# Optimization experiments

Measured on AMD Instinct MI355X. Metric: run time of the kernel, lower is better.

The kernel has to match this reference:

```python
import jax, jax.numpy as jnp
import numpy as np
import math

H = 1024      # hidden_size
NH = 16       # num_attention_heads
HD = H // NH  # head_dim = 64
FF = 4096     # intermediate_size
AD = 256      # adapter_hidden_size
NB = 320      # num_buckets
MAXD = 800    # max_bucket_distance
B = 4
S = 1024
EPS = 1e-5


def _rel_bucket(rel):
    # HF WavLM _relative_positions_bucket
    nb = NB // 2
    buckets = (rel > 0).astype(jnp.int32) * nb
    rel = jnp.abs(rel)
    max_exact = nb // 2
    is_small = rel < max_exact
    large = max_exact + (
        jnp.log(jnp.maximum(rel, 1).astype(jnp.float32) / max_exact)
        / math.log(MAXD / max_exact) * (nb - max_exact)
    ).astype(jnp.int32)
    large = jnp.minimum(large, nb - 1)
    return buckets + jnp.where(is_small, rel, large)


def _ln(x, g, b):
    m = x.mean(-1, keepdims=True)
    v = ((x - m) ** 2).mean(-1, keepdims=True)
    return (x - m) * jax.lax.rsqrt(v + EPS) * g + b


def setup_inputs() -> dict:
    key = jax.random.key(0)
    ks = jax.random.split(key, 12)
    sc = 0.02
    w = lambda k, shape: jax.random.normal(k, shape, jnp.float32) * sc
    return dict(
        x=jax.random.normal(ks[0], (B, S, H), jnp.float32),
        Wq=w(ks[1], (H, H)), bq=jnp.zeros((H,), jnp.float32),
        Wk=w(ks[2], (H, H)), bk=jnp.zeros((H,), jnp.float32),
        Wv=w(ks[3], (H, H)), bv=jnp.zeros((H,), jnp.float32),
        Wo=w(ks[4], (H, H)), bo=jnp.zeros((H,), jnp.float32),
        Wg=w(ks[5], (8, HD)), bg=jnp.zeros((8,), jnp.float32),
        gru_const=jnp.ones((1, NH, 1, 1), jnp.float32),
        rel_embed=w(ks[6], (NB, NH)),
        ln1_g=jnp.ones((H,), jnp.float32), ln1_b=jnp.zeros((H,), jnp.float32),
        W1=w(ks[7], (FF, H)), b1=jnp.zeros((FF,), jnp.float32),
        W2=w(ks[8], (H, FF)), b2=jnp.zeros((H,), jnp.float32),
        ln2_g=jnp.ones((H,), jnp.float32), ln2_b=jnp.zeros((H,), jnp.float32),
        Wad=w(ks[9], (AD, H)), bad=jnp.zeros((AD,), jnp.float32),
        Wau=w(ks[10], (H, AD)), bau=jnp.zeros((H,), jnp.float32),
    )


def reference(x, Wq, bq, Wk, bk, Wv, bv, Wo, bo, Wg, bg, gru_const, rel_embed,
              ln1_g, ln1_b, W1, b1, W2, b2, ln2_g, ln2_b, Wad, bad, Wau, bau):
    b, s, _ = x.shape
    # --- relative position bias (first layer: position_bias=None) ---
    pos = jnp.arange(s)
    rel = pos[None, :] - pos[:, None]                 # memory - context
    pos_bias = rel_embed[_rel_bucket(rel)].transpose(2, 0, 1)  # (nh, s, s)

    # --- GRU-style gating of the bias (per batch, head, query pos) ---
    xh = x.reshape(b, s, NH, HD).transpose(0, 2, 1, 3)         # (b, nh, s, hd)
    gproj = jnp.einsum('bhsd,ed->bhse', xh, Wg) + bg           # (b, nh, s, 8)
    gproj = gproj.reshape(b, NH, s, 2, 4).sum(-1)              # (b, nh, s, 2)
    gate = jax.nn.sigmoid(gproj)
    gate_a, gate_b = gate[..., 0:1], gate[..., 1:2]            # (b, nh, s, 1)
    gate_out = gate_a * (gate_b * gru_const - 1.0) + 2.0       # (b, nh, s, 1)
    gated_bias = gate_out * pos_bias[None]                     # (b, nh, s, s)

    # --- multi-head self-attention with additive gated bias ---
    q = (x @ Wq.T + bq).reshape(b, s, NH, HD)
    k = (x @ Wk.T + bk).reshape(b, s, NH, HD)
    v = (x @ Wv.T + bv).reshape(b, s, NH, HD)
    scores = jnp.einsum('bihd,bjhd->bhij', q, k) * (HD ** -0.5) + gated_bias
    attn = jax.nn.softmax(scores, axis=-1)
    ctx = jnp.einsum('bhij,bjhd->bihd', attn, v).reshape(b, s, H)
    attn_out = ctx @ Wo.T + bo

    # --- residual + LN, FFN + adapter (idx_without_adapter=None path) + LN ---
    h = _ln(x + attn_out, ln1_g, ln1_b)
    ff = jax.nn.gelu(h @ W1.T + b1, approximate=False) @ W2.T + b2
    adapt = jax.nn.elu(h @ Wad.T + bad) @ Wau.T + bau
    h = h + ff + adapt
    return _ln(h, ln2_g, ln2_b)
```

## Files before the change

kernel.cpp:

```cpp
#include <hip/hip_runtime.h>
#include <cmath>

typedef unsigned short u16;
using short8 = __attribute__((ext_vector_type(8))) short;
using f32x4  = __attribute__((ext_vector_type(4))) float;

__device__ __forceinline__ u16 f2bf(float f) {
  union { float f; unsigned u; } c; c.f = f;
  unsigned r = c.u + 0x7fffu + ((c.u >> 16) & 1u);
  return (u16)(r >> 16);
}

__device__ __forceinline__ void gld_lds16(void* lds, const void* g) {
  __builtin_amdgcn_global_load_lds(
      (const __attribute__((address_space(1))) void*)g,
      (__attribute__((address_space(3))) void*)lds, 16, 0, 0);
}

__global__ __launch_bounds__(256) void cvt_bf16(const float* __restrict__ in,
                                                u16* __restrict__ out, int n4) {
  int i = blockIdx.x * 256 + threadIdx.x;
  if (i >= n4) return;
  float4 v = ((const float4*)in)[i];
  ushort4 o;
  o.x = f2bf(v.x); o.y = f2bf(v.y); o.z = f2bf(v.z); o.w = f2bf(v.w);
  ((ushort4*)out)[i] = o;
}

__global__ __launch_bounds__(256) void btab_kernel(const float* __restrict__ rel_embed,
                                                   float* __restrict__ btab) {
  int idx = blockIdx.x * 256 + threadIdx.x;
  if (idx >= 16 * 2048) return;
  int h = idx >> 11;
  int d = idx & 2047;
  if (d >= 2047) return;
  int rel = d - 1023;
  int bucket = (rel > 0) ? 160 : 0;
  int ar = rel < 0 ? -rel : rel;
  if (ar < 80) {
    bucket += ar;
  } else {
    int large = 80 + (int)(logf((float)ar / 80.0f) / 2.3025851f * 80.0f);
    if (large > 159) large = 159;
    bucket += large;
  }
  btab[h * 2048 + d] = rel_embed[bucket * 16 + h];
}

__global__ __launch_bounds__(256) void gate_kernel(const float* __restrict__ x,
                                                   const float* __restrict__ Wg,
                                                   const float* __restrict__ bg,
                                                   const float* __restrict__ gc,
                                                   float* __restrict__ gate_out) {
  int gw = blockIdx.x * 4 + (threadIdx.x >> 6);
  int lane = threadIdx.x & 63;
  int s = gw & 1023, bh = gw >> 10, b = bh >> 4, h = bh & 15;
  float wA = Wg[lane] + Wg[64 + lane] + Wg[128 + lane] + Wg[192 + lane];
  float wB = Wg[256 + lane] + Wg[320 + lane] + Wg[384 + lane] + Wg[448 + lane];
  float xv = x[((size_t)(b * 1024 + s)) * 1024 + h * 64 + lane];
  float pa = xv * wA, pb = xv * wB;
  #pragma unroll
  for (int m = 1; m < 64; m <<= 1) {
    pa += __shfl_xor(pa, m, 64);
    pb += __shfl_xor(pb, m, 64);
  }
  if (lane == 0) {
    float bgA = bg[0] + bg[1] + bg[2] + bg[3];
    float bgB = bg[4] + bg[5] + bg[6] + bg[7];
    float ga = 1.f / (1.f + expf(-(pa + bgA)));
    float gb = 1.f / (1.f + expf(-(pb + bgB)));
    gate_out[(size_t)bh * 1024 + s] = ga * (gb * gc[h] - 1.f) + 2.f;
  }
}

template <int MODE>
__global__ __launch_bounds__(256) void gemm_bt(
    const u16* __restrict__ A, const u16* __restrict__ Bw,
    int M, int N, int K,
    const float* __restrict__ bias0, const float* __restrict__ bias1,
    const float* __restrict__ bias2, const float* __restrict__ resid,
    float* __restrict__ outf,
    u16* __restrict__ ob0, u16* __restrict__ ob1, u16* __restrict__ ob2) {
  __shared__ __align__(16) u16 As[128 * 32];
  __shared__ __align__(16) u16 Bs[128 * 32];
  const int tid = threadIdx.x;
  const int lane = tid & 63, wave = tid >> 6;
  const int quad = lane >> 4, l16 = lane & 15;
  const int bm = blockIdx.y * 128, bn = blockIdx.x * 128;
  const int wm = (wave & 1) * 64, wn = (wave >> 1) * 64;
  const int srow = lane >> 2;
  const int scol = (lane & 3) * 8;

  f32x4 acc[4][4] = {};

  for (int k0 = 0; k0 < K; k0 += 32) {
    #pragma unroll
    for (int it = 0; it < 2; ++it) {
      int rbase = (it * 4 + wave) * 16;
      gld_lds16(&As[rbase * 32], &A[(size_t)(bm + rbase + srow) * K + k0 + scol]);
      gld_lds16(&Bs[rbase * 32], &Bw[(size_t)(bn + rbase + srow) * K + k0 + scol]);
    }
    __syncthreads();
    short8 af[4], bf[4];
    #pragma unroll
    for (int mi = 0; mi < 4; ++mi)
      af[mi] = *(const short8*)&As[(wm + mi * 16 + l16) * 32 + quad * 8];
    #pragma unroll
    for (int ni = 0; ni < 4; ++ni)
      bf[ni] = *(const short8*)&Bs[(wn + ni * 16 + l16) * 32 + quad * 8];
    #pragma unroll
    for (int mi = 0; mi < 4; ++mi)
      #pragma unroll
      for (int ni = 0; ni < 4; ++ni)
        acc[mi][ni] = __builtin_amdgcn_mfma_f32_16x16x32_bf16(af[mi], bf[ni], acc[mi][ni], 0, 0, 0);
    __syncthreads();
  }

  #pragma unroll
  for (int mi = 0; mi < 4; ++mi) {
    #pragma unroll
    for (int ni = 0; ni < 4; ++ni) {
      int col = bn + wn + ni * 16 + l16;
      #pragma unroll
      for (int r = 0; r < 4; ++r) {
        int m = bm + wm + mi * 16 + quad * 4 + r;
        float v = acc[mi][ni][r];
        if constexpr (MODE == 0) {
          int seg = col >> 10;
          int nloc = col & 1023;
          const float* bs = seg == 0 ? bias0 : (seg == 1 ? bias1 : bias2);
          u16* dst = seg == 0 ? ob0 : (seg == 1 ? ob1 : ob2);
          v += bs[nloc];
          if (seg == 0) v *= 0.125f;
          dst[(size_t)m * 1024 + nloc] = f2bf(v);
        } else if constexpr (MODE == 1) {
          v += bias0[col] + resid[(size_t)m * N + col];
          outf[(size_t)m * N + col] = v;
        } else {
          if (col < 4096) {
            float t = v + bias0[col];
            float g = 0.5f * t * (1.f + erff(t * 0.70710678118f));
            ob0[(size_t)m * 4096 + col] = f2bf(g);
          } else {
            int nloc = col - 4096;
            float t = v + bias1[nloc];
            float e = t > 0.f ? t : expm1f(t);
            ob1[(size_t)m * 256 + nloc] = f2bf(e);
          }
        }
      }
    }
  }
}

__global__ __launch_bounds__(256) void attn_kernel(
    const u16* __restrict__ qb, const u16* __restrict__ kb, const u16* __restrict__ vb,
    const float* __restrict__ gate, const float* __restrict__ btab,
    u16* __restrict__ ctxb) {
  __shared__ __align__(16) u16 Qs[64 * 64];
  __shared__ __align__(16) u16 Ks[64 * 64];
  __shared__ __align__(16) u16 Vt[64 * 72];
  __shared__ __align__(16) u16 Ps[4][16 * 72];
  __shared__ float btl[2047];
  __shared__ float gbuf[64];

  const int tid = threadIdx.x;
  const int lane = tid & 63, wave = tid >> 6;
  const int quad = lane >> 4, l16 = lane & 15;
  const int it0 = blockIdx.x * 64;
  const int bh = blockIdx.y, b = bh >> 4, h = bh & 15;

  for (int idx = tid; idx < 2047; idx += 256) btl[idx] = btab[h * 2048 + idx];
  if (tid < 64) gbuf[tid] = gate[(size_t)bh * 1024 + it0 + tid];

  {
    int r = tid >> 3, c = (tid & 7) * 8;
    #pragma unroll
    for (int p = 0; p < 2; ++p) {
      int row = p * 32 + r;
      *(uint4*)&Qs[row * 64 + c] =
          *(const uint4*)&qb[((size_t)(b * 1024 + it0 + row)) * 1024 + h * 64 + c];
    }
  }

  f32x4 oacc[4] = {};
  float mrow[4], lrow[4];
  #pragma unroll
  for (int r = 0; r < 4; ++r) { mrow[r] = -1e30f; lrow[r] = 0.f; }

  __syncthreads();

  for (int jt = 0; jt < 16; ++jt) {
    int j0 = jt * 64;
    {
      int r = tid >> 3, c = (tid & 7) * 8;
      #pragma unroll
      for (int p = 0; p < 2; ++p) {
        int row = p * 32 + r;
        size_t gidx = ((size_t)(b * 1024 + j0 + row)) * 1024 + h * 64 + c;
        *(uint4*)&Ks[row * 64 + c] = *(const uint4*)&kb[gidx];
        uint4 vv = *(const uint4*)&vb[gidx];
        const u16* pv = (const u16*)&vv;
        #pragma unroll
        for (int e = 0; e < 8; ++e) Vt[(c + e) * 72 + row] = pv[e];
      }
    }
    __syncthreads();

    f32x4 sacc[4] = {};
    #pragma unroll
    for (int c = 0; c < 2; ++c) {
      short8 aq = *(const short8*)&Qs[(wave * 16 + l16) * 64 + c * 32 + quad * 8];
      #pragma unroll
      for (int nt = 0; nt < 4; ++nt) {
        short8 bk8 = *(const short8*)&Ks[(nt * 16 + l16) * 64 + c * 32 + quad * 8];
        sacc[nt] = __builtin_amdgcn_mfma_f32_16x16x32_bf16(aq, bk8, sacc[nt], 0, 0, 0);
      }
    }

    float sc[4][4], mt[4];
    #pragma unroll
    for (int r = 0; r < 4; ++r) {
      int i_loc = wave * 16 + quad * 4 + r;
      int i_glob = it0 + i_loc;
      float g = gbuf[i_loc];
      float mx = -1e30f;
      #pragma unroll
      for (int nt = 0; nt < 4; ++nt) {
        int j = j0 + nt * 16 + l16;
        float s = sacc[nt][r] + g * btl[j - i_glob + 1023];
        sc[nt][r] = s;
        mx = fmaxf(mx, s);
      }
      mt[r] = mx;
    }
    #pragma unroll
    for (int m = 1; m < 16; m <<= 1)
      #pragma unroll
      for (int r = 0; r < 4; ++r) mt[r] = fmaxf(mt[r], __shfl_xor(mt[r], m, 64));

    float alpha[4], ls[4];
    #pragma unroll
    for (int r = 0; r < 4; ++r) {
      float mnew = fmaxf(mrow[r], mt[r]);
      alpha[r] = expf(mrow[r] - mnew);
      mrow[r] = mnew;
      float lsum = 0.f;
      #pragma unroll
      for (int nt = 0; nt < 4; ++nt) {
        float p = expf(sc[nt][r] - mnew);
        sc[nt][r] = p;
        lsum += p;
      }
      ls[r] = lsum;
    }
    #pragma unroll
    for (int m = 1; m < 16; m <<= 1)
      #pragma unroll
      for (int r = 0; r < 4; ++r) ls[r] += __shfl_xor(ls[r], m, 64);
    #pragma unroll
    for (int r = 0; r < 4; ++r) lrow[r] = lrow[r] * alpha[r] + ls[r];

    #pragma unroll
    for (int nt = 0; nt < 4; ++nt)
      #pragma unroll
      for (int r = 0; r < 4; ++r)
        Ps[wave][(quad * 4 + r) * 72 + nt * 16 + l16] = f2bf(sc[nt][r]);

    #pragma unroll
    for (int dt = 0; dt < 4; ++dt)
      #pragma unroll
      for (int r = 0; r < 4; ++r) oacc[dt][r] *= alpha[r];

    #pragma unroll
    for (int c = 0; c < 2; ++c) {
      short8 ap = *(const short8*)&Ps[wave][l16 * 72 + c * 32 + quad * 8];
      #pragma unroll
      for (int dt = 0; dt < 4; ++dt) {
        short8 bv8 = *(const short8*)&Vt[(dt * 16 + l16) * 72 + c * 32 + quad * 8];
        oacc[dt] = __builtin_amdgcn_mfma_f32_16x16x32_bf16(ap, bv8, oacc[dt], 0, 0, 0);
      }
    }
    __syncthreads();
  }

  #pragma unroll
  for (int dt = 0; dt < 4; ++dt)
    #pragma unroll
    for (int r = 0; r < 4; ++r) {
      int i_loc = wave * 16 + quad * 4 + r;
      int d = dt * 16 + l16;
      float o = oacc[dt][r] / lrow[r];
      ctxb[((size_t)(b * 1024 + it0 + i_loc)) * 1024 + h * 64 + d] = f2bf(o);
    }
}

template <bool WRITE_BF16>
__global__ __launch_bounds__(256) void ln_kernel(const float* __restrict__ in,
                                                 const float* __restrict__ g,
                                                 const float* __restrict__ bta,
                                                 float* __restrict__ outf,
                                                 u16* __restrict__ outb) {
  __shared__ float red[8];
  int row = blockIdx.x, tid = threadIdx.x;
  int lane = tid & 63, wave = tid >> 6;
  const float* p = in + (size_t)row * 1024;
  float4 v = *(const float4*)&p[tid * 4];
  float s = v.x + v.y + v.z + v.w;
  #pragma unroll
  for (int m = 1; m < 64; m <<= 1) s += __shfl_xor(s, m, 64);
  if (lane == 0) red[wave] = s;
  __syncthreads();
  float mean = (red[0] + red[1] + red[2] + red[3]) * (1.f / 1024.f);
  float d0 = v.x - mean, d1 = v.y - mean, d2 = v.z - mean, d3 = v.w - mean;
  float sq = d0 * d0 + d1 * d1 + d2 * d2 + d3 * d3;
  #pragma unroll
  for (int m = 1; m < 64; m <<= 1) sq += __shfl_xor(sq, m, 64);
  if (lane == 0) red[4 + wave] = sq;
  __syncthreads();
  float var = (red[4] + red[5] + red[6] + red[7]) * (1.f / 1024.f);
  float rstd = rsqrtf(var + 1e-5f);
  float dd[4] = {d0, d1, d2, d3};
  #pragma unroll
  for (int e = 0; e < 4; ++e) {
    int cidx = tid * 4 + e;
    float val = dd[e] * rstd * g[cidx] + bta[cidx];
    outf[(size_t)row * 1024 + cidx] = val;
    if (WRITE_BF16) outb[(size_t)row * 1024 + cidx] = f2bf(val);
  }
}

extern "C" void kernel_launch(void* const* d_in, const int* in_sizes, int n_in,
                              void* d_out, int out_size, void* d_ws, size_t ws_size,
                              hipStream_t stream) {
  const float* x    = (const float*)d_in[0];
  const float* Wq   = (const float*)d_in[1];  const float* bq  = (const float*)d_in[2];
  const float* Wk   = (const float*)d_in[3];  const float* bk  = (const float*)d_in[4];
  const float* Wv   = (const float*)d_in[5];  const float* bv  = (const float*)d_in[6];
  const float* Wo   = (const float*)d_in[7];  const float* bo  = (const float*)d_in[8];
  const float* Wg   = (const float*)d_in[9];  const float* bg  = (const float*)d_in[10];
  const float* gc   = (const float*)d_in[11];
  const float* rel  = (const float*)d_in[12];
  const float* ln1g = (const float*)d_in[13]; const float* ln1b = (const float*)d_in[14];
  const float* W1   = (const float*)d_in[15]; const float* b1  = (const float*)d_in[16];
  const float* W2   = (const float*)d_in[17]; const float* b2  = (const float*)d_in[18];
  const float* ln2g = (const float*)d_in[19]; const float* ln2b = (const float*)d_in[20];
  const float* Wad  = (const float*)d_in[21]; const float* bad = (const float*)d_in[22];
  const float* Wau  = (const float*)d_in[23]; const float* bau = (const float*)d_in[24];
  float* out = (float*)d_out;

  char* ws = (char*)d_ws;
  const size_t MB = 1ull << 20;
  u16*   xb   = (u16*)(ws + 0 * MB);
  u16*   wqkv = (u16*)(ws + 8 * MB);
  u16*   wob  = (u16*)(ws + 14 * MB);
  u16*   w1ad = (u16*)(ws + 16 * MB);
  u16*   w2b  = (u16*)(ws + 25 * MB);
  u16*   waub = (u16*)(ws + 33 * MB);
  u16*   qb   = (u16*)(ws + 34 * MB);
  u16*   kb   = (u16*)(ws + 42 * MB);
  u16*   vbp  = (u16*)(ws + 50 * MB);
  float* gate = (float*)(ws + 58 * MB);
  float* btab = (float*)(ws + 58 * MB + 262144);
  u16*   ctxb = (u16*)(ws + 59 * MB);
  float* ares = (float*)(ws + 67 * MB);
  float* hf   = (float*)(ws + 83 * MB);
  u16*   hb   = (u16*)(ws + 99 * MB);
  u16*   ffb  = (u16*)(ws + 34 * MB);
  u16*   adp  = (u16*)(ws + 107 * MB);
  float* y    = (float*)(ws + 67 * MB);
  (void)ws_size; (void)n_in; (void)in_sizes; (void)out_size;

  auto cvt = [&](const float* src, u16* dst, int n) {
    cvt_bf16<<<(n / 4 + 255) / 256, 256, 0, stream>>>(src, dst, n / 4);
  };
  cvt(x, xb, 4096 * 1024);
  cvt(Wq, wqkv,               1024 * 1024);
  cvt(Wk, wqkv + 1024 * 1024, 1024 * 1024);
  cvt(Wv, wqkv + 2 * 1024 * 1024, 1024 * 1024);
  cvt(Wo, wob, 1024 * 1024);
  cvt(W1, w1ad, 4096 * 1024);
  cvt(Wad, w1ad + 4096 * 1024, 256 * 1024);
  cvt(W2, w2b, 4096 * 1024);
  cvt(Wau, waub, 1024 * 256);

  btab_kernel<<<128, 256, 0, stream>>>(rel, btab);
  gate_kernel<<<16384, 256, 0, stream>>>(x, Wg, bg, gc, gate);

  gemm_bt<0><<<dim3(24, 32), 256, 0, stream>>>(xb, wqkv, 4096, 3072, 1024,
      bq, bk, bv, nullptr, nullptr, qb, kb, vbp);
  attn_kernel<<<dim3(16, 64), 256, 0, stream>>>(qb, kb, vbp, gate, btab, ctxb);
  gemm_bt<1><<<dim3(8, 32), 256, 0, stream>>>(ctxb, wob, 4096, 1024, 1024,
      bo, nullptr, nullptr, x, ares, nullptr, nullptr, nullptr);
  ln_kernel<true><<<4096, 256, 0, stream>>>(ares, ln1g, ln1b, hf, hb);
  gemm_bt<2><<<dim3(34, 32), 256, 0, stream>>>(hb, w1ad, 4096, 4352, 1024,
      b1, bad, nullptr, nullptr, nullptr, ffb, adp, nullptr);
  gemm_bt<1><<<dim3(8, 32), 256, 0, stream>>>(ffb, w2b, 4096, 1024, 4096,
      b2, nullptr, nullptr, hf, y, nullptr, nullptr, nullptr);
  gemm_bt<1><<<dim3(8, 32), 256, 0, stream>>>(adp, waub, 4096, 1024, 256,
      bau, nullptr, nullptr, y, y, nullptr, nullptr, nullptr);
  ln_kernel<false><<<4096, 256, 0, stream>>>(y, ln2g, ln2b, out, nullptr);
}
```

Baseline: 594.9 us.

## Use MFMA-fragment LDS layout, pre-transpose V, async loads in attention

Changes the LDS tile layout in the GEMM and attention kernels so each 16-row slab is stored in MFMA fragment order, which avoids bank conflicts on the short8 reads. Adds a separate kernel that transposes V into a per-head d-major buffer, so attention can stream K, V and Q straight into LDS with global_load_lds instead of doing a scalar scatter-transpose on every tile. The attention kernel also stores the bias table as bf16 and switches to fast __expf, trading some precision and an extra launch plus a round trip through global memory for V.

```diff
diff --git a/kernel.cpp b/kernel.cpp
--- a/kernel.cpp
+++ b/kernel.cpp
@@ -9,6 +9,10 @@
   union { float f; unsigned u; } c; c.f = f;
   unsigned r = c.u + 0x7fffu + ((c.u >> 16) & 1u);
   return (u16)(r >> 16);
+}
+__device__ __forceinline__ float bf2f(u16 b) {
+  union { unsigned u; float f; } c; c.u = ((unsigned)b) << 16;
+  return c.f;
 }
 
 __device__ __forceinline__ void gld_lds16(void* lds, const void* g) {
@@ -73,6 +77,32 @@
   }
 }
 
+__global__ __launch_bounds__(256) void vtrans_kernel(const u16* __restrict__ vb,
+                                                     u16* __restrict__ vt) {
+  __shared__ u16 tile[64 * 65];
+  int bh = blockIdx.y, b = bh >> 4, h = bh & 15;
+  int s0 = blockIdx.x * 64;
+  int tid = threadIdx.x;
+  int r = tid >> 3, c = (tid & 7) * 8;
+  #pragma unroll
+  for (int p = 0; p < 2; ++p) {
+    int s = p * 32 + r;
+    uint4 vv = *(const uint4*)&vb[((size_t)(b * 1024 + s0 + s)) * 1024 + h * 64 + c];
+    const u16* pv = (const u16*)&vv;
+    #pragma unroll
+    for (int e = 0; e < 8; ++e) tile[(c + e) * 65 + s] = pv[e];
+  }
+  __syncthreads();
+  int d = tid & 63, jc0 = tid >> 6;
+  #pragma unroll
+  for (int jc = jc0; jc < 8; jc += 4) {
+    u16 tmp[8];
+    #pragma unroll
+    for (int e = 0; e < 8; ++e) tmp[e] = tile[d * 65 + jc * 8 + e];
+    *(uint4*)&vt[((size_t)(bh * 64 + d)) * 1024 + s0 + jc * 8] = *(uint4*)tmp;
+  }
+}
+
 template <int MODE>
 __global__ __launch_bounds__(256) void gemm_bt(
     const u16* __restrict__ A, const u16* __restrict__ Bw,
@@ -88,26 +118,26 @@
   const int quad = lane >> 4, l16 = lane & 15;
   const int bm = blockIdx.y * 128, bn = blockIdx.x * 128;
   const int wm = (wave & 1) * 64, wn = (wave >> 1) * 64;
-  const int srow = lane >> 2;
-  const int scol = (lane & 3) * 8;
+  const int sr = lane & 15;
+  const int skc = (lane >> 4) * 8;
 
   f32x4 acc[4][4] = {};
 
   for (int k0 = 0; k0 < K; k0 += 32) {
     #pragma unroll
-    for (int it = 0; it < 2; ++it) {
-      int rbase = (it * 4 + wave) * 16;
-      gld_lds16(&As[rbase * 32], &A[(size_t)(bm + rbase + srow) * K + k0 + scol]);
-      gld_lds16(&Bs[rbase * 32], &Bw[(size_t)(bn + rbase + srow) * K + k0 + scol]);
+    for (int t = 0; t < 2; ++t) {
+      int s = wave * 2 + t;
+      gld_lds16(&As[s * 512], &A[(size_t)(bm + s * 16 + sr) * K + k0 + skc]);
+      gld_lds16(&Bs[s * 512], &Bw[(size_t)(bn + s * 16 + sr) * K + k0 + skc]);
     }
     __syncthreads();
     short8 af[4], bf[4];
     #pragma unroll
     for (int mi = 0; mi < 4; ++mi)
-      af[mi] = *(const short8*)&As[(wm + mi * 16 + l16) * 32 + quad * 8];
+      af[mi] = *(const short8*)&As[((wm >> 4) + mi) * 512 + quad * 128 + l16 * 8];
     #pragma unroll
     for (int ni = 0; ni < 4; ++ni)
-      bf[ni] = *(const short8*)&Bs[(wn + ni * 16 + l16) * 32 + quad * 8];
+      bf[ni] = *(const short8*)&Bs[((wn >> 4) + ni) * 512 + quad * 128 + l16 * 8];
     #pragma unroll
     for (int mi = 0; mi < 4; ++mi)
       #pragma unroll
@@ -154,14 +184,14 @@
 }
 
 __global__ __launch_bounds__(256) void attn_kernel(
-    const u16* __restrict__ qb, const u16* __restrict__ kb, const u16* __restrict__ vb,
+    const u16* __restrict__ qb, const u16* __restrict__ kb, const u16* __restrict__ vt,
     const float* __restrict__ gate, const float* __restrict__ btab,
     u16* __restrict__ ctxb) {
   __shared__ __align__(16) u16 Qs[64 * 64];
   __shared__ __align__(16) u16 Ks[64 * 64];
-  __shared__ __align__(16) u16 Vt[64 * 72];
-  __shared__ __align__(16) u16 Ps[4][16 * 72];
-  __shared__ float btl[2047];
+  __shared__ __align__(16) u16 Vs[64 * 64];
+  __shared__ __align__(16) u16 Ps[4][16 * 64];
+  __shared__ u16 btl[2048];
   __shared__ float gbuf[64];
 
   const int tid = threadIdx.x;
@@ -169,19 +199,16 @@
   const int quad = lane >> 4, l16 = lane & 15;
   const int it0 = blockIdx.x * 64;
   const int bh = blockIdx.y, b = bh >> 4, h = bh & 15;
-
-  for (int idx = tid; idx < 2047; idx += 256) btl[idx] = btab[h * 2048 + idx];
+  const int sr = lane & 15;
+  const int skc = (lane >> 4) * 8;
+
+  for (int idx = tid; idx < 2047; idx += 256) btl[idx] = f2bf(btab[h * 2048 + idx]);
   if (tid < 64) gbuf[tid] = gate[(size_t)bh * 1024 + it0 + tid];
 
-  {
-    int r = tid >> 3, c = (tid & 7) * 8;
-    #pragma unroll
-    for (int p = 0; p < 2; ++p) {
-      int row = p * 32 + r;
-      *(uint4*)&Qs[row * 64 + c] =
-          *(const uint4*)&qb[((size_t)(b * 1024 + it0 + row)) * 1024 + h * 64 + c];
-    }
-  }
+  #pragma unroll
+  for (int hf = 0; hf < 2; ++hf)
+    gld_lds16(&Qs[wave * 1024 + hf * 512],
+              &qb[((size_t)(b * 1024 + it0 + wave * 16 + sr)) * 1024 + h * 64 + hf * 32 + skc]);
 
   f32x4 oacc[4] = {};
   float mrow[4], lrow[4];
@@ -192,28 +219,22 @@
 
   for (int jt = 0; jt < 16; ++jt) {
     int j0 = jt * 64;
-    {
-      int r = tid >> 3, c = (tid & 7) * 8;
-      #pragma unroll
-      for (int p = 0; p < 2; ++p) {
-        int row = p * 32 + r;
-        size_t gidx = ((size_t)(b * 1024 + j0 + row)) * 1024 + h * 64 + c;
-        *(uint4*)&Ks[row * 64 + c] = *(const uint4*)&kb[gidx];
-        uint4 vv = *(const uint4*)&vb[gidx];
-        const u16* pv = (const u16*)&vv;
-        #pragma unroll
-        for (int e = 0; e < 8; ++e) Vt[(c + e) * 72 + row] = pv[e];
-      }
+    #pragma unroll
+    for (int hf = 0; hf < 2; ++hf) {
+      gld_lds16(&Ks[wave * 1024 + hf * 512],
+                &kb[((size_t)(b * 1024 + j0 + wave * 16 + sr)) * 1024 + h * 64 + hf * 32 + skc]);
+      gld_lds16(&Vs[wave * 1024 + hf * 512],
+                &vt[((size_t)(bh * 64 + wave * 16 + sr)) * 1024 + j0 + hf * 32 + skc]);
     }
     __syncthreads();
 
     f32x4 sacc[4] = {};
     #pragma unroll
     for (int c = 0; c < 2; ++c) {
-      short8 aq = *(const short8*)&Qs[(wave * 16 + l16) * 64 + c * 32 + quad * 8];
+      short8 aq = *(const short8*)&Qs[wave * 1024 + (c * 4 + quad) * 128 + l16 * 8];
       #pragma unroll
       for (int nt = 0; nt < 4; ++nt) {
-        short8 bk8 = *(const short8*)&Ks[(nt * 16 + l16) * 64 + c * 32 + quad * 8];
+        short8 bk8 = *(const short8*)&Ks[nt * 1024 + (c * 4 + quad) * 128 + l16 * 8];
         sacc[nt] = __builtin_amdgcn_mfma_f32_16x16x32_bf16(aq, bk8, sacc[nt], 0, 0, 0);
       }
     }
@@ -228,7 +249,7 @@
       #pragma unroll
       for (int nt = 0; nt < 4; ++nt) {
         int j = j0 + nt * 16 + l16;
-        float s = sacc[nt][r] + g * btl[j - i_glob + 1023];
+        float s = sacc[nt][r] + g * bf2f(btl[j - i_glob + 1023]);
         sc[nt][r] = s;
         mx = fmaxf(mx, s);
       }
@@ -243,12 +264,12 @@
     #pragma unroll
     for (int r = 0; r < 4; ++r) {
       float mnew = fmaxf(mrow[r], mt[r]);
-      alpha[r] = expf(mrow[r] - mnew);
+      alpha[r] = __expf(mrow[r] - mnew);
       mrow[r] = mnew;
       float lsum = 0.f;
       #pragma unroll
       for (int nt = 0; nt < 4; ++nt) {
-        float p = expf(sc[nt][r] - mnew);
+        float p = __expf(sc[nt][r] - mnew);
         sc[nt][r] = p;
         lsum += p;
       }
@@ -265,7 +286,7 @@
     for (int nt = 0; nt < 4; ++nt)
       #pragma unroll
       for (int r = 0; r < 4; ++r)
-        Ps[wave][(quad * 4 + r) * 72 + nt * 16 + l16] = f2bf(sc[nt][r]);
+        Ps[wave][(nt * 2 + (l16 >> 3)) * 128 + (quad * 4 + r) * 8 + (l16 & 7)] = f2bf(sc[nt][r]);
 
     #pragma unroll
     for (int dt = 0; dt < 4; ++dt)
@@ -274,10 +295,10 @@
 
     #pragma unroll
     for (int c = 0; c < 2; ++c) {
-      short8 ap = *(const short8*)&Ps[wave][l16 * 72 + c * 32 + quad * 8];
+      short8 ap = *(const short8*)&Ps[wave][(c * 4 + quad) * 128 + l16 * 8];
       #pragma unroll
       for (int dt = 0; dt < 4; ++dt) {
-        short8 bv8 = *(const short8*)&Vt[(dt * 16 + l16) * 72 + c * 32 + quad * 8];
+        short8 bv8 = *(const short8*)&Vs[dt * 1024 + (c * 4 + quad) * 128 + l16 * 8];
         oacc[dt] = __builtin_amdgcn_mfma_f32_16x16x32_bf16(ap, bv8, oacc[dt], 0, 0, 0);
       }
     }
@@ -368,6 +389,7 @@
   u16*   hb   = (u16*)(ws + 99 * MB);
   u16*   ffb  = (u16*)(ws + 34 * MB);
   u16*   adp  = (u16*)(ws + 107 * MB);
+  u16*   vtb  = (u16*)(ws + 109 * MB);
   float* y    = (float*)(ws + 67 * MB);
   (void)ws_size; (void)n_in; (void)in_sizes; (void)out_size;
 
@@ -389,7 +411,8 @@
 
   gemm_bt<0><<<dim3(24, 32), 256, 0, stream>>>(xb, wqkv, 4096, 3072, 1024,
       bq, bk, bv, nullptr, nullptr, qb, kb, vbp);
-  attn_kernel<<<dim3(16, 64), 256, 0, stream>>>(qb, kb, vbp, gate, btab, ctxb);
+  vtrans_kernel<<<dim3(16, 64), 256, 0, stream>>>(vbp, vtb);
+  attn_kernel<<<dim3(16, 64), 256, 0, stream>>>(qb, kb, vtb, gate, btab, ctxb);
   gemm_bt<1><<<dim3(8, 32), 256, 0, stream>>>(ctxb, wob, 4096, 1024, 1024,
       bo, nullptr, nullptr, x, ares, nullptr, nullptr, nullptr);
   ln_kernel<true><<<4096, 256, 0, stream>>>(ares, ln1g, ln1b, hf, hb);
```

Result: slower. 633.5 us (+6.5%).
